# Performance work log

Hardware: AMD Instinct MI355X
Metric: run time of the kernel (lower is better)

Reference implementation:

```python
import jax, jax.numpy as jnp
import numpy as np


def _conv1x1(w, b, x):
    # 1x1 Conv2d == channel matmul: w [O,C], x [B,C,H,W] -> [B,O,H,W]
    return jnp.einsum('oc,bchw->bohw', w, x) + b[None, :, None, None]


def setup_inputs() -> dict:
    key = jax.random.key(0)
    ks = jax.random.split(key, 9)
    C = 512
    B, H, W = 8, 32, 32
    s = 0.02
    return {
        'x': jax.random.normal(ks[0], (B, C, H, W), dtype=jnp.float32),
        'wq': jax.random.normal(ks[1], (C, C), dtype=jnp.float32) * s,
        'bq': jax.random.normal(ks[2], (C,), dtype=jnp.float32) * s,
        'wk': jax.random.normal(ks[3], (C, C), dtype=jnp.float32) * s,
        'bk': jax.random.normal(ks[4], (C,), dtype=jnp.float32) * s,
        'wv': jax.random.normal(ks[5], (C, C), dtype=jnp.float32) * s,
        'bv': jax.random.normal(ks[6], (C,), dtype=jnp.float32) * s,
        'wo': jax.random.normal(ks[7], (C, C), dtype=jnp.float32) * s,
        'bo': jax.random.normal(ks[8], (C,), dtype=jnp.float32) * s,
        'heads': 8,
    }


def reference(x, wq, bq, wk, bk, wv, bv, wo, bo, heads):
    B, C, H, W = x.shape
    N = H * W
    d = C // heads
    scale = jnp.asarray(d, x.dtype) ** 0.5

    vx = _conv1x1(wv, bv, x)                       # value(x), reused for residual
    Q = _conv1x1(wq, bq, x).reshape(B, heads, d, N)
    K = _conv1x1(wk, bk, x).reshape(B, heads, d, N)
    V = vx.reshape(B, heads, d, N)

    attn = jax.nn.softmax(jnp.einsum('bhcn,bhcm->bhnm', Q, K) / scale, axis=-1)
    attn_out = jnp.einsum('bhnm,bhcm->bhcn', attn, V).reshape(B, C, H, W)

    out = attn_out + vx                            # residual uses value(x)
    return _conv1x1(wo, bo, out)
```

## Files before the change

### kernel.cpp

```cpp
#include <hip/hip_runtime.h>
#include <cstdint>
#include <cmath>

#define B_ 8
#define C_ 512
#define N_ 1024
#define H_ 8
#define D_ 64


using u16 = unsigned short;

typedef __bf16 bf16x8 __attribute__((ext_vector_type(8)));
typedef float  f32x4  __attribute__((ext_vector_type(4)));
typedef unsigned short us8 __attribute__((ext_vector_type(8)));

#if __has_builtin(__builtin_amdgcn_exp2f)
#define EXP2(x) __builtin_amdgcn_exp2f(x)
#else
#define EXP2(x) exp2f(x)
#endif

#define QSCALE 0.1803368801111244f


__device__ __forceinline__ float b2f(u16 u) {
    return __uint_as_float(((uint32_t)u) << 16);
}
__device__ __forceinline__ u16 f2b(float f) {
    uint32_t x = __float_as_uint(f);
    return (u16)((x + 0x7fffu + ((x >> 16) & 1u)) >> 16);
}
__device__ __forceinline__ u16 f2bt(float f) {
    return (u16)(__float_as_uint(f) >> 16);
}
__device__ __forceinline__ float sf(float f) {
    return (fabsf(f) < 1e30f) ? f : 0.0f;
}
__device__ __forceinline__ u16 sf2b(float f) { return f2b(sf(f)); }

template<bool WB>
__device__ __forceinline__ us8 ldw(const void* W, size_t idx) {
    if constexpr (WB) {
        return *(const us8*)((const u16*)W + idx);
    } else {
        const float* p = (const float*)W + idx;
        float4 a = *(const float4*)p, b = *(const float4*)(p + 4);
        us8 pk;
        pk[0] = sf2b(a.x); pk[1] = sf2b(a.y); pk[2] = sf2b(a.z); pk[3] = sf2b(a.w);
        pk[4] = sf2b(b.x); pk[5] = sf2b(b.y); pk[6] = sf2b(b.z); pk[7] = sf2b(b.w);
        return pk;
    }
}


__global__ __launch_bounds__(256) void k_pre(const float* __restrict__ x,
                                             u16* __restrict__ xt,
                                             const float* __restrict__ wq,
                                             const float* __restrict__ wk,
                                             const float* __restrict__ wv,
                                             const float* __restrict__ wo,
                                             u16* __restrict__ wb) {
    const int tid = threadIdx.x;
    const int nb = blockIdx.x, cb = blockIdx.y, b = blockIdx.z;
    if (b == 8) {
        if (wb == nullptr) return;
        int base = (cb * 16 + nb) * 256 + tid;
#pragma unroll
        for (int i = 0; i < 8; ++i) {
            int idx = base + i * 32768;
            int m = idx >> 16;
            int off = (idx & 65535) << 2;
            const float* src = (m == 0) ? wq : (m == 1) ? wk : (m == 2) ? wv : wo;
            float4 v = *(const float4*)&src[off];
            ushort4 w;
            w.x = sf2b(v.x); w.y = sf2b(v.y); w.z = sf2b(v.z); w.w = sf2b(v.w);
            *(ushort4*)&wb[(m << 18) + off] = w;
        }
        return;
    }
    __shared__ __align__(16) u16 t[64][72];
#pragma unroll
    for (int i = 0; i < 4; ++i) {
        int q = tid + i * 256;
        int row = q >> 4, cg = q & 15;
        float4 v = *(const float4*)&x[((size_t)(b * C_ + cb * 64 + row) << 10) + nb * 64 + cg * 4];
        ushort4 w;
        w.x = sf2b(v.x); w.y = sf2b(v.y); w.z = sf2b(v.z); w.w = sf2b(v.w);
        *(ushort4*)&t[row][cg * 4] = w;
    }
    __syncthreads();
#pragma unroll
    for (int i = 0; i < 4; ++i) {
        int q = tid + i * 256;
        int nrow = q >> 4, cg = q & 15;
        ushort4 w;
        w.x = t[cg * 4 + 0][nrow];
        w.y = t[cg * 4 + 1][nrow];
        w.z = t[cg * 4 + 2][nrow];
        w.w = t[cg * 4 + 3][nrow];
        *(ushort4*)&xt[((size_t)(b * N_ + nb * 64 + nrow) << 9) + cb * 64 + cg * 4] = w;
    }
}


template<bool WB>
__global__ __launch_bounds__(256) void k_proj_t(
    const u16* __restrict__ xt,
    const void* __restrict__ wq, const float* __restrict__ bq,
    const void* __restrict__ wk, const float* __restrict__ bk,
    const void* __restrict__ wv, const float* __restrict__ bv,
    u16* __restrict__ qt, u16* __restrict__ kt,
    u16* __restrict__ v,  u16* __restrict__ vxt) {
    __shared__ __align__(16) u16 lA[128 * 64];
    __shared__ __align__(16) u16 lB[128 * 64];
    const int tid = threadIdx.x;
    const int op = blockIdx.z >> 3, b = blockIdx.z & 7;
    const int n0 = blockIdx.x * 128, o0 = blockIdx.y * 128;
    const void*  W  = (op == 0) ? wq : (op == 1) ? wk : wv;
    const float* BI = (op == 0) ? bq : (op == 1) ? bk : bv;
    const u16* A = xt + ((size_t)b << 19);
    const int lane = tid & 63, wave = tid >> 6;
    const int wm = (wave >> 1) * 64, wn = (wave & 1) * 64;
    const int l15 = lane & 15, lg = lane >> 4;
    const int xs = (l15 & 7) << 3;

    f32x4 acc[4][4];
    const f32x4 vzero = {0.f, 0.f, 0.f, 0.f};
#pragma unroll
    for (int i = 0; i < 4; ++i)
#pragma unroll
        for (int j = 0; j < 4; ++j) acc[i][j] = vzero;

    us8 ra[4], rwB[4];
    auto loadk = [&](int k0) {
#pragma unroll
        for (int p = 0; p < 4; ++p) {
            int slot = p * 256 + tid;
            int row = slot >> 3, seg = slot & 7;
            ra[p] = *(const us8*)&A[(size_t)(n0 + row) * C_ + k0 + seg * 8];
            rwB[p] = ldw<WB>(W, (size_t)(o0 + row) * C_ + k0 + seg * 8);
        }
    };
    loadk(0);

    for (int k0 = 0; k0 < C_; k0 += 64) {
        __syncthreads();
#pragma unroll
        for (int p = 0; p < 4; ++p) {
            int slot = p * 256 + tid;
            int row = slot >> 3, seg = slot & 7;
            int off = row * 64 + ((seg ^ (row & 7)) << 3);
            *(us8*)&lA[off] = ra[p];
            *(us8*)&lB[off] = rwB[p];
        }
        if (k0 + 64 < C_) loadk(k0 + 64);
        __syncthreads();
#pragma unroll
        for (int kk = 0; kk < 64; kk += 32) {
            const int col = (kk + lg * 8) ^ xs;
            bf16x8 af[4], bfr[4];
#pragma unroll
            for (int i = 0; i < 4; ++i)
                af[i] = *(const bf16x8*)&lA[(wm + i * 16 + l15) * 64 + col];
#pragma unroll
            for (int j = 0; j < 4; ++j)
                bfr[j] = *(const bf16x8*)&lB[(wn + j * 16 + l15) * 64 + col];
#pragma unroll
            for (int i = 0; i < 4; ++i)
#pragma unroll
                for (int j = 0; j < 4; ++j)
                    acc[i][j] = __builtin_amdgcn_mfma_f32_16x16x32_bf16(af[i], bfr[j], acc[i][j], 0, 0, 0);
        }
    }

    if (op < 2) {
        u16* outp = (op == 0) ? qt : kt;
        const float scl = (op == 0) ? QSCALE : 1.0f;
#pragma unroll
        for (int i = 0; i < 4; ++i) {
            int nb2 = n0 + wm + i * 16 + lg * 4;
#pragma unroll
            for (int j = 0; j < 4; ++j) {
                int o = o0 + wn + j * 16 + l15;
                float bias = sf(BI[o]);
                int h = o >> 6, dl = o & 63;
                size_t base = ((size_t)b * H_ + h) << 10;
#pragma unroll
                for (int r = 0; r < 4; ++r)
                    outp[(base + nb2 + r) * D_ + dl] = f2b((acc[i][j][r] + bias) * scl);
            }
        }
    } else {
#pragma unroll
        for (int i = 0; i < 4; ++i) {
            int nb2 = n0 + wm + i * 16 + lg * 4;
#pragma unroll
            for (int j = 0; j < 4; ++j) {
                int o = o0 + wn + j * 16 + l15;
                float bias = sf(BI[o]);
                float p0 = acc[i][j][0] + bias, p1 = acc[i][j][1] + bias;
                float p2 = acc[i][j][2] + bias, p3 = acc[i][j][3] + bias;
                ushort4 pk; pk.x = f2b(p0); pk.y = f2b(p1); pk.z = f2b(p2); pk.w = f2b(p3);
                *(ushort4*)&v[((size_t)(b * C_ + o) << 10) + nb2] = pk;
                vxt[((size_t)(b * N_ + nb2 + 0) << 9) + o] = pk.x;
                vxt[((size_t)(b * N_ + nb2 + 1) << 9) + o] = pk.y;
                vxt[((size_t)(b * N_ + nb2 + 2) << 9) + o] = pk.z;
                vxt[((size_t)(b * N_ + nb2 + 3) << 9) + o] = pk.w;
            }
        }
    }
}


__global__ __launch_bounds__(256, 4) void k_attn(
    const u16* __restrict__ qt, const u16* __restrict__ kt,
    const u16* __restrict__ v,  const u16* __restrict__ vxt,
    u16* __restrict__ rt) {
    __shared__ __align__(16) u16 lK[64 * 64];
    __shared__ __align__(16) u16 lV[64 * 64];
    __shared__ __align__(16) u16 lP[4][32 * 64];
    const int tid = threadIdx.x, lane = tid & 63, wave = tid >> 6;
    const int l15 = lane & 15, lg = lane >> 4;
    const int xs = (l15 & 7) << 3;
    const int bid = blockIdx.x;
    const int qb = bid >> 6, bh = bid & 63;
    const int b = bh >> 3, h = bh & 7;
    const size_t bh_off = (size_t)bh << 16;
    const int q0 = qb * 128;
    const int nA = wave * 32;

    bf16x8 qf[2][2];
#pragma unroll
    for (int nt = 0; nt < 2; ++nt)
#pragma unroll
        for (int k = 0; k < 2; ++k)
            qf[nt][k] = *(const bf16x8*)&qt[bh_off +
                (size_t)(q0 + nA + nt * 16 + l15) * D_ + k * 32 + lg * 8];

    us8 rk[2], rv[2];
    auto loadkv = [&](int mb) {
#pragma unroll
        for (int p = 0; p < 2; ++p) {
            int slot = p * 256 + tid;
            int row = slot >> 3, seg = slot & 7;
            rk[p] = *(const us8*)&kt[bh_off + (size_t)(mb * 64 + row) * D_ + seg * 8];
            rv[p] = *(const us8*)&v[((size_t)(b * C_ + h * 64 + row) << 10) + mb * 64 + seg * 8];
        }
    };
    loadkv(0);

    float L[2] = {0.f, 0.f};
    f32x4 oacc[2][4];
    const f32x4 vzero = {0.f, 0.f, 0.f, 0.f};
#pragma unroll
    for (int nt = 0; nt < 2; ++nt)
#pragma unroll
        for (int ct = 0; ct < 4; ++ct) oacc[nt][ct] = vzero;

    for (int mb = 0; mb < 16; ++mb) {
        __syncthreads();
#pragma unroll
        for (int p = 0; p < 2; ++p) {
            int slot = p * 256 + tid;
            int row = slot >> 3, seg = slot & 7;
            int off = row * 64 + ((seg ^ (row & 7)) << 3);
            *(us8*)&lK[off] = rk[p];
            *(us8*)&lV[off] = rv[p];
        }
        if (mb < 15) loadkv(mb + 1);
        __syncthreads();

        f32x4 s[4][2];
#pragma unroll
        for (int mt = 0; mt < 4; ++mt)
#pragma unroll
            for (int nt = 0; nt < 2; ++nt) s[mt][nt] = vzero;
#pragma unroll
        for (int k = 0; k < 2; ++k) {
            const int col = (k * 32 + lg * 8) ^ xs;
            bf16x8 aK[4];
#pragma unroll
            for (int mt = 0; mt < 4; ++mt)
                aK[mt] = *(const bf16x8*)&lK[(mt * 16 + l15) * 64 + col];
            __builtin_amdgcn_s_setprio(1);
#pragma unroll
            for (int mt = 0; mt < 4; ++mt)
#pragma unroll
                for (int nt = 0; nt < 2; ++nt)
                    s[mt][nt] = __builtin_amdgcn_mfma_f32_16x16x32_bf16(aK[mt], qf[nt][k], s[mt][nt], 0, 0, 0);
            __builtin_amdgcn_s_setprio(0);
        }

#pragma unroll
        for (int mt = 0; mt < 4; ++mt)
#pragma unroll
            for (int nt = 0; nt < 2; ++nt) {
                float p0 = EXP2(s[mt][nt][0]);
                float p1 = EXP2(s[mt][nt][1]);
                float p2 = EXP2(s[mt][nt][2]);
                float p3 = EXP2(s[mt][nt][3]);
                L[nt] += p0 + p1 + p2 + p3;
                ushort4 pk; pk.x = f2bt(p0); pk.y = f2bt(p1); pk.z = f2bt(p2); pk.w = f2bt(p3);
                *(ushort4*)&lP[wave][(nt * 16 + l15) * 64 + ((mt * 16 + lg * 4) ^ xs)] = pk;
            }

#pragma unroll
        for (int kk2 = 0; kk2 < 64; kk2 += 32) {
            const int colv = (kk2 + lg * 8) ^ xs;
            bf16x8 aP[2], bV[4];
#pragma unroll
            for (int nt = 0; nt < 2; ++nt)
                aP[nt] = *(const bf16x8*)&lP[wave][(nt * 16 + l15) * 64 + colv];
#pragma unroll
            for (int ct = 0; ct < 4; ++ct)
                bV[ct] = *(const bf16x8*)&lV[(ct * 16 + l15) * 64 + colv];
            __builtin_amdgcn_s_setprio(1);
#pragma unroll
            for (int nt = 0; nt < 2; ++nt)
#pragma unroll
                for (int ct = 0; ct < 4; ++ct)
                    oacc[nt][ct] = __builtin_amdgcn_mfma_f32_16x16x32_bf16(aP[nt], bV[ct], oacc[nt][ct], 0, 0, 0);
            __builtin_amdgcn_s_setprio(0);
        }
    }

#pragma unroll
    for (int nt = 0; nt < 2; ++nt) {
        float s2 = L[nt];
        s2 += __shfl_xor(s2, 16);
        s2 += __shfl_xor(s2, 32);
        L[nt] = s2;
    }

#pragma unroll
    for (int nt = 0; nt < 2; ++nt) {
        float inv[4];
#pragma unroll
        for (int r = 0; r < 4; ++r) inv[r] = 1.0f / __shfl(L[nt], lg * 4 + r);
#pragma unroll
        for (int ct = 0; ct < 4; ++ct) {
            int ch = h * 64 + ct * 16 + l15;
#pragma unroll
            for (int r = 0; r < 4; ++r) {
                int n = q0 + nA + nt * 16 + lg * 4 + r;
                size_t idx = ((size_t)(b * N_ + n) << 9) + ch;
                rt[idx] = f2b(oacc[nt][ct][r] * inv[r] + b2f(vxt[idx]));
            }
        }
    }
}


template<bool WB>
__global__ __launch_bounds__(256) void k_out_t(
    const u16* __restrict__ rt, const void* __restrict__ wo,
    const float* __restrict__ bo, float* __restrict__ out) {
    __shared__ __align__(16) u16 lA[128 * 64];
    __shared__ __align__(16) u16 lB[128 * 64];
    const int tid = threadIdx.x;
    const int b = blockIdx.z;
    const int n0 = blockIdx.x * 128, o0 = blockIdx.y * 128;
    const u16* Rb = rt + ((size_t)b << 19);
    const int lane = tid & 63, wave = tid >> 6;
    const int wm = (wave >> 1) * 64, wn = (wave & 1) * 64;
    const int l15 = lane & 15, lg = lane >> 4;
    const int xs = (l15 & 7) << 3;

    f32x4 acc[4][4];
    const f32x4 vzero = {0.f, 0.f, 0.f, 0.f};
#pragma unroll
    for (int i = 0; i < 4; ++i)
#pragma unroll
        for (int j = 0; j < 4; ++j) acc[i][j] = vzero;

    us8 rb[4], rwB[4];
    auto loadk = [&](int k0) {
#pragma unroll
        for (int p = 0; p < 4; ++p) {
            int slot = p * 256 + tid;
            int row = slot >> 3, seg = slot & 7;
            rwB[p] = ldw<WB>(wo, (size_t)(o0 + row) * C_ + k0 + seg * 8);
            rb[p] = *(const us8*)&Rb[(size_t)(n0 + row) * C_ + k0 + seg * 8];
        }
    };
    loadk(0);

    for (int k0 = 0; k0 < C_; k0 += 64) {
        __syncthreads();
#pragma unroll
        for (int p = 0; p < 4; ++p) {
            int slot = p * 256 + tid;
            int row = slot >> 3, seg = slot & 7;
            int off = row * 64 + ((seg ^ (row & 7)) << 3);
            *(us8*)&lA[off] = rwB[p];
            *(us8*)&lB[off] = rb[p];
        }
        if (k0 + 64 < C_) loadk(k0 + 64);
        __syncthreads();
#pragma unroll
        for (int kk = 0; kk < 64; kk += 32) {
            const int col = (kk + lg * 8) ^ xs;
            bf16x8 af[4], bfr[4];
#pragma unroll
            for (int i = 0; i < 4; ++i)
                af[i] = *(const bf16x8*)&lA[(wm + i * 16 + l15) * 64 + col];
#pragma unroll
            for (int j = 0; j < 4; ++j)
                bfr[j] = *(const bf16x8*)&lB[(wn + j * 16 + l15) * 64 + col];
#pragma unroll
            for (int i = 0; i < 4; ++i)
#pragma unroll
                for (int j = 0; j < 4; ++j)
                    acc[i][j] = __builtin_amdgcn_mfma_f32_16x16x32_bf16(af[i], bfr[j], acc[i][j], 0, 0, 0);
        }
    }

#pragma unroll
    for (int i = 0; i < 4; ++i) {
#pragma unroll
        for (int j = 0; j < 4; ++j) {
            int nn = n0 + wn + j * 16 + l15;
#pragma unroll
            for (int r = 0; r < 4; ++r) {
                int o = o0 + wm + i * 16 + lg * 4 + r;
                out[((size_t)(b * C_ + o) << 10) + nn] = acc[i][j][r] + sf(bo[o]);
            }
        }
    }
}


extern "C" void kernel_launch(void* const* d_in, const int* in_sizes, int n_in,
                              void* d_out, int out_size, void* d_ws, size_t ws_size,
                              hipStream_t stream) {
    const float* x  = (const float*)d_in[0];
    const float* wq = (const float*)d_in[1];
    const float* bq = (const float*)d_in[2];
    const float* wk = (const float*)d_in[3];
    const float* bk = (const float*)d_in[4];
    const float* wv = (const float*)d_in[5];
    const float* bv = (const float*)d_in[6];
    const float* wo = (const float*)d_in[7];
    const float* bo = (const float*)d_in[8];
    float* out = (float*)d_out;
    u16* ws = (u16*)d_ws;

    const size_t T = (size_t)B_ * C_ * N_;
    const size_t WSZ = (size_t)4 * C_ * C_;
    if (ws_size < 5 * T * sizeof(u16)) return;

    u16* xt  = ws;
    u16* qt  = ws + 1 * T;
    u16* kt  = ws + 2 * T;
    u16* vv  = ws + 3 * T;
    u16* vxt = ws + 4 * T;
    u16* rt  = xt;
    u16* wb  = ws + 5 * T;

    const bool wbfit = ws_size >= (5 * T + WSZ) * sizeof(u16);

    k_pre<<<dim3(16, 8, 9), 256, 0, stream>>>(x, xt, wq, wk, wv, wo,
                                              wbfit ? wb : (u16*)nullptr);
    if (wbfit) {
        k_proj_t<true><<<dim3(8, 4, 24), 256, 0, stream>>>(
            xt, wb, bq, wb + 262144, bk, wb + 524288, bv, qt, kt, vv, vxt);
    } else {
        k_proj_t<false><<<dim3(8, 4, 24), 256, 0, stream>>>(
            xt, wq, bq, wk, bk, wv, bv, qt, kt, vv, vxt);
    }
    k_attn<<<dim3(512), 256, 0, stream>>>(qt, kt, vv, vxt, rt);
    if (wbfit) {
        k_out_t<true><<<dim3(8, 4, 8), 256, 0, stream>>>(rt, wb + 786432, bo, out);
    } else {
        k_out_t<false><<<dim3(8, 4, 8), 256, 0, stream>>>(rt, wo, bo, out);
    }
}
```

Before: 78.99 us.

## Use direct global-to-LDS loads and double-buffer K/V tiles in attention

Replaces register-staged global loads and LDS stores with global_load_lds direct-to-LDS transfers in the projection GEMMs (bf16 weight path) and the attention kernel. The swizzle is moved into the global source address. The attention kernel double-buffers K/V tiles so the next block is fetched while the current one is computed, with one barrier per iteration. Occupancy is lowered to 3 blocks per CU to fit the extra LDS. The GEMM bf16 path loses its register prefetch overlap, since the load is issued and waited on within the same iteration.

```diff
diff --git a/kernel.cpp b/kernel.cpp
--- a/kernel.cpp
+++ b/kernel.cpp
@@ -39,18 +39,20 @@
 }
 __device__ __forceinline__ u16 sf2b(float f) { return f2b(sf(f)); }
 
-template<bool WB>
-__device__ __forceinline__ us8 ldw(const void* W, size_t idx) {
-    if constexpr (WB) {
-        return *(const us8*)((const u16*)W + idx);
-    } else {
-        const float* p = (const float*)W + idx;
-        float4 a = *(const float4*)p, b = *(const float4*)(p + 4);
-        us8 pk;
-        pk[0] = sf2b(a.x); pk[1] = sf2b(a.y); pk[2] = sf2b(a.z); pk[3] = sf2b(a.w);
-        pk[4] = sf2b(b.x); pk[5] = sf2b(b.y); pk[6] = sf2b(b.z); pk[7] = sf2b(b.w);
-        return pk;
-    }
+__device__ __forceinline__ void gl16(const void* g, const void* l) {
+    __builtin_amdgcn_global_load_lds(
+        (const __attribute__((address_space(1))) uint32_t*)g,
+        (__attribute__((address_space(3))) uint32_t*)(uint32_t)(uintptr_t)l,
+        16, 0, 0);
+}
+
+__device__ __forceinline__ us8 ldwf(const float* W, size_t idx) {
+    const float* p = W + idx;
+    float4 a = *(const float4*)p, b = *(const float4*)(p + 4);
+    us8 pk;
+    pk[0] = sf2b(a.x); pk[1] = sf2b(a.y); pk[2] = sf2b(a.z); pk[3] = sf2b(a.w);
+    pk[4] = sf2b(b.x); pk[5] = sf2b(b.y); pk[6] = sf2b(b.z); pk[7] = sf2b(b.w);
+    return pk;
 }
 
 
@@ -139,22 +141,35 @@
             int slot = p * 256 + tid;
             int row = slot >> 3, seg = slot & 7;
             ra[p] = *(const us8*)&A[(size_t)(n0 + row) * C_ + k0 + seg * 8];
-            rwB[p] = ldw<WB>(W, (size_t)(o0 + row) * C_ + k0 + seg * 8);
+            rwB[p] = ldwf((const float*)W, (size_t)(o0 + row) * C_ + k0 + seg * 8);
         }
     };
-    loadk(0);
+    if constexpr (!WB) loadk(0);
 
     for (int k0 = 0; k0 < C_; k0 += 64) {
         __syncthreads();
-#pragma unroll
-        for (int p = 0; p < 4; ++p) {
-            int slot = p * 256 + tid;
-            int row = slot >> 3, seg = slot & 7;
-            int off = row * 64 + ((seg ^ (row & 7)) << 3);
-            *(us8*)&lA[off] = ra[p];
-            *(us8*)&lB[off] = rwB[p];
-        }
-        if (k0 + 64 < C_) loadk(k0 + 64);
+        if constexpr (WB) {
+            const u16* W16 = (const u16*)W;
+#pragma unroll
+            for (int p = 0; p < 4; ++p) {
+                int slot = p * 256 + tid;
+                int row = slot >> 3;
+                int segs = (slot & 7) ^ (row & 7);
+                int lb = (p * 256 + (tid & 192)) * 8;
+                gl16(&A[(size_t)(n0 + row) * C_ + k0 + segs * 8], &lA[lb]);
+                gl16(&W16[(size_t)(o0 + row) * C_ + k0 + segs * 8], &lB[lb]);
+            }
+        } else {
+#pragma unroll
+            for (int p = 0; p < 4; ++p) {
+                int slot = p * 256 + tid;
+                int row = slot >> 3, seg = slot & 7;
+                int off = row * 64 + ((seg ^ (row & 7)) << 3);
+                *(us8*)&lA[off] = ra[p];
+                *(us8*)&lB[off] = rwB[p];
+            }
+            if (k0 + 64 < C_) loadk(k0 + 64);
+        }
         __syncthreads();
 #pragma unroll
         for (int kk = 0; kk < 64; kk += 32) {
@@ -213,12 +228,12 @@
 }
 
 
-__global__ __launch_bounds__(256, 4) void k_attn(
+__global__ __launch_bounds__(256, 3) void k_attn(
     const u16* __restrict__ qt, const u16* __restrict__ kt,
     const u16* __restrict__ v,  const u16* __restrict__ vxt,
     u16* __restrict__ rt) {
-    __shared__ __align__(16) u16 lK[64 * 64];
-    __shared__ __align__(16) u16 lV[64 * 64];
+    __shared__ __align__(16) u16 lK[2][64 * 64];
+    __shared__ __align__(16) u16 lV[2][64 * 64];
     __shared__ __align__(16) u16 lP[4][32 * 64];
     const int tid = threadIdx.x, lane = tid & 63, wave = tid >> 6;
     const int l15 = lane & 15, lg = lane >> 4;
@@ -238,17 +253,19 @@
             qf[nt][k] = *(const bf16x8*)&qt[bh_off +
                 (size_t)(q0 + nA + nt * 16 + l15) * D_ + k * 32 + lg * 8];
 
-    us8 rk[2], rv[2];
-    auto loadkv = [&](int mb) {
+    auto stage = [&](int mb, int buf) {
 #pragma unroll
         for (int p = 0; p < 2; ++p) {
             int slot = p * 256 + tid;
-            int row = slot >> 3, seg = slot & 7;
-            rk[p] = *(const us8*)&kt[bh_off + (size_t)(mb * 64 + row) * D_ + seg * 8];
-            rv[p] = *(const us8*)&v[((size_t)(b * C_ + h * 64 + row) << 10) + mb * 64 + seg * 8];
+            int row = slot >> 3;
+            int segs = (slot & 7) ^ (row & 7);
+            int lb = (p * 256 + (tid & 192)) * 8;
+            gl16(&kt[bh_off + (size_t)(mb * 64 + row) * D_ + segs * 8], &lK[buf][lb]);
+            gl16(&v[((size_t)(b * C_ + h * 64 + row) << 10) + mb * 64 + segs * 8], &lV[buf][lb]);
         }
     };
-    loadkv(0);
+    stage(0, 0);
+    __syncthreads();
 
     float L[2] = {0.f, 0.f};
     f32x4 oacc[2][4];
@@ -259,17 +276,10 @@
         for (int ct = 0; ct < 4; ++ct) oacc[nt][ct] = vzero;
 
     for (int mb = 0; mb < 16; ++mb) {
-        __syncthreads();
-#pragma unroll
-        for (int p = 0; p < 2; ++p) {
-            int slot = p * 256 + tid;
-            int row = slot >> 3, seg = slot & 7;
-            int off = row * 64 + ((seg ^ (row & 7)) << 3);
-            *(us8*)&lK[off] = rk[p];
-            *(us8*)&lV[off] = rv[p];
-        }
-        if (mb < 15) loadkv(mb + 1);
-        __syncthreads();
+        const int cur = mb & 1;
+        if (mb < 15) stage(mb + 1, cur ^ 1);
+        const u16* lKc = lK[cur];
+        const u16* lVc = lV[cur];
 
         f32x4 s[4][2];
 #pragma unroll
@@ -282,7 +292,7 @@
             bf16x8 aK[4];
 #pragma unroll
             for (int mt = 0; mt < 4; ++mt)
-                aK[mt] = *(const bf16x8*)&lK[(mt * 16 + l15) * 64 + col];
+                aK[mt] = *(const bf16x8*)&lKc[(mt * 16 + l15) * 64 + col];
             __builtin_amdgcn_s_setprio(1);
 #pragma unroll
             for (int mt = 0; mt < 4; ++mt)
@@ -314,7 +324,7 @@
                 aP[nt] = *(const bf16x8*)&lP[wave][(nt * 16 + l15) * 64 + colv];
 #pragma unroll
             for (int ct = 0; ct < 4; ++ct)
-                bV[ct] = *(const bf16x8*)&lV[(ct * 16 + l15) * 64 + colv];
+                bV[ct] = *(const bf16x8*)&lVc[(ct * 16 + l15) * 64 + colv];
             __builtin_amdgcn_s_setprio(1);
 #pragma unroll
             for (int nt = 0; nt < 2; ++nt)
@@ -323,6 +333,8 @@
                     oacc[nt][ct] = __builtin_amdgcn_mfma_f32_16x16x32_bf16(aP[nt], bV[ct], oacc[nt][ct], 0, 0, 0);
             __builtin_amdgcn_s_setprio(0);
         }
+
+        __syncthreads();
     }
 
 #pragma unroll
@@ -380,23 +392,36 @@
         for (int p = 0; p < 4; ++p) {
             int slot = p * 256 + tid;
             int row = slot >> 3, seg = slot & 7;
-            rwB[p] = ldw<WB>(wo, (size_t)(o0 + row) * C_ + k0 + seg * 8);
+            rwB[p] = ldwf((const float*)wo, (size_t)(o0 + row) * C_ + k0 + seg * 8);
             rb[p] = *(const us8*)&Rb[(size_t)(n0 + row) * C_ + k0 + seg * 8];
         }
     };
-    loadk(0);
+    if constexpr (!WB) loadk(0);
 
     for (int k0 = 0; k0 < C_; k0 += 64) {
         __syncthreads();
-#pragma unroll
-        for (int p = 0; p < 4; ++p) {
-            int slot = p * 256 + tid;
-            int row = slot >> 3, seg = slot & 7;
-            int off = row * 64 + ((seg ^ (row & 7)) << 3);
-            *(us8*)&lA[off] = rwB[p];
-            *(us8*)&lB[off] = rb[p];
-        }
-        if (k0 + 64 < C_) loadk(k0 + 64);
+        if constexpr (WB) {
+            const u16* W16 = (const u16*)wo;
+#pragma unroll
+            for (int p = 0; p < 4; ++p) {
+                int slot = p * 256 + tid;
+                int row = slot >> 3;
+                int segs = (slot & 7) ^ (row & 7);
+                int lb = (p * 256 + (tid & 192)) * 8;
+                gl16(&W16[(size_t)(o0 + row) * C_ + k0 + segs * 8], &lA[lb]);
+                gl16(&Rb[(size_t)(n0 + row) * C_ + k0 + segs * 8], &lB[lb]);
+            }
+        } else {
+#pragma unroll
+            for (int p = 0; p < 4; ++p) {
+                int slot = p * 256 + tid;
+                int row = slot >> 3, seg = slot & 7;
+                int off = row * 64 + ((seg ^ (row & 7)) << 3);
+                *(us8*)&lA[off] = rwB[p];
+                *(us8*)&lB[off] = rb[p];
+            }
+            if (k0 + 64 < C_) loadk(k0 + 64);
+        }
         __syncthreads();
 #pragma unroll
         for (int kk = 0; kk < 64; kk += 32) {
```

New measurement: 76.31 us. 1.04x faster.

## Drop transposed V copy, read K/V directly from global, vectorize output stores

Applied to the files above, without the earlier changes.

Removes the separate transposed value buffer (vxt) and its scattered 2-byte stores in the projection kernel, reading the residual from the channel-major V buffer instead. The attention kernel stops staging K and V tiles through shared memory with barriers and loads MFMA fragments straight from global memory, relying on cache reuse across the four waves. The output projection swaps operand roles so each lane writes a contiguous float4 per channel instead of scalar strided stores. Dropping the LDS staging removes syncs and LDS traffic but makes every wave issue its own global loads for K/V, which may raise latency exposure.

```diff
diff --git a/kernel.cpp b/kernel.cpp
--- a/kernel.cpp
+++ b/kernel.cpp
@@ -111,7 +111,7 @@
     const void* __restrict__ wk, const float* __restrict__ bk,
     const void* __restrict__ wv, const float* __restrict__ bv,
     u16* __restrict__ qt, u16* __restrict__ kt,
-    u16* __restrict__ v,  u16* __restrict__ vxt) {
+    u16* __restrict__ v) {
     __shared__ __align__(16) u16 lA[128 * 64];
     __shared__ __align__(16) u16 lB[128 * 64];
     const int tid = threadIdx.x;
@@ -199,26 +199,21 @@
             for (int j = 0; j < 4; ++j) {
                 int o = o0 + wn + j * 16 + l15;
                 float bias = sf(BI[o]);
-                float p0 = acc[i][j][0] + bias, p1 = acc[i][j][1] + bias;
-                float p2 = acc[i][j][2] + bias, p3 = acc[i][j][3] + bias;
-                ushort4 pk; pk.x = f2b(p0); pk.y = f2b(p1); pk.z = f2b(p2); pk.w = f2b(p3);
+                ushort4 pk;
+                pk.x = f2b(acc[i][j][0] + bias);
+                pk.y = f2b(acc[i][j][1] + bias);
+                pk.z = f2b(acc[i][j][2] + bias);
+                pk.w = f2b(acc[i][j][3] + bias);
                 *(ushort4*)&v[((size_t)(b * C_ + o) << 10) + nb2] = pk;
-                vxt[((size_t)(b * N_ + nb2 + 0) << 9) + o] = pk.x;
-                vxt[((size_t)(b * N_ + nb2 + 1) << 9) + o] = pk.y;
-                vxt[((size_t)(b * N_ + nb2 + 2) << 9) + o] = pk.z;
-                vxt[((size_t)(b * N_ + nb2 + 3) << 9) + o] = pk.w;
             }
         }
     }
 }
 
 
-__global__ __launch_bounds__(256, 4) void k_attn(
+__global__ __launch_bounds__(256) void k_attn(
     const u16* __restrict__ qt, const u16* __restrict__ kt,
-    const u16* __restrict__ v,  const u16* __restrict__ vxt,
-    u16* __restrict__ rt) {
-    __shared__ __align__(16) u16 lK[64 * 64];
-    __shared__ __align__(16) u16 lV[64 * 64];
+    const u16* __restrict__ v, u16* __restrict__ rt) {
     __shared__ __align__(16) u16 lP[4][32 * 64];
     const int tid = threadIdx.x, lane = tid & 63, wave = tid >> 6;
     const int l15 = lane & 15, lg = lane >> 4;
@@ -238,17 +233,8 @@
             qf[nt][k] = *(const bf16x8*)&qt[bh_off +
                 (size_t)(q0 + nA + nt * 16 + l15) * D_ + k * 32 + lg * 8];
 
-    us8 rk[2], rv[2];
-    auto loadkv = [&](int mb) {
-#pragma unroll
-        for (int p = 0; p < 2; ++p) {
-            int slot = p * 256 + tid;
-            int row = slot >> 3, seg = slot & 7;
-            rk[p] = *(const us8*)&kt[bh_off + (size_t)(mb * 64 + row) * D_ + seg * 8];
-            rv[p] = *(const us8*)&v[((size_t)(b * C_ + h * 64 + row) << 10) + mb * 64 + seg * 8];
-        }
-    };
-    loadkv(0);
+    const u16* Kb = kt + bh_off;
+    const u16* Vb = v + ((size_t)(b * C_ + h * 64) << 10);
 
     float L[2] = {0.f, 0.f};
     f32x4 oacc[2][4];
@@ -259,18 +245,6 @@
         for (int ct = 0; ct < 4; ++ct) oacc[nt][ct] = vzero;
 
     for (int mb = 0; mb < 16; ++mb) {
-        __syncthreads();
-#pragma unroll
-        for (int p = 0; p < 2; ++p) {
-            int slot = p * 256 + tid;
-            int row = slot >> 3, seg = slot & 7;
-            int off = row * 64 + ((seg ^ (row & 7)) << 3);
-            *(us8*)&lK[off] = rk[p];
-            *(us8*)&lV[off] = rv[p];
-        }
-        if (mb < 15) loadkv(mb + 1);
-        __syncthreads();
-
         f32x4 s[4][2];
 #pragma unroll
         for (int mt = 0; mt < 4; ++mt)
@@ -278,11 +252,10 @@
             for (int nt = 0; nt < 2; ++nt) s[mt][nt] = vzero;
 #pragma unroll
         for (int k = 0; k < 2; ++k) {
-            const int col = (k * 32 + lg * 8) ^ xs;
             bf16x8 aK[4];
 #pragma unroll
             for (int mt = 0; mt < 4; ++mt)
-                aK[mt] = *(const bf16x8*)&lK[(mt * 16 + l15) * 64 + col];
+                aK[mt] = *(const bf16x8*)&Kb[(size_t)(mb * 64 + mt * 16 + l15) * D_ + k * 32 + lg * 8];
             __builtin_amdgcn_s_setprio(1);
 #pragma unroll
             for (int mt = 0; mt < 4; ++mt)
@@ -314,7 +287,7 @@
                 aP[nt] = *(const bf16x8*)&lP[wave][(nt * 16 + l15) * 64 + colv];
 #pragma unroll
             for (int ct = 0; ct < 4; ++ct)
-                bV[ct] = *(const bf16x8*)&lV[(ct * 16 + l15) * 64 + colv];
+                bV[ct] = *(const bf16x8*)&Vb[((size_t)(ct * 16 + l15) << 10) + mb * 64 + kk2 + lg * 8];
             __builtin_amdgcn_s_setprio(1);
 #pragma unroll
             for (int nt = 0; nt < 2; ++nt)
@@ -341,11 +314,13 @@
 #pragma unroll
         for (int ct = 0; ct < 4; ++ct) {
             int ch = h * 64 + ct * 16 + l15;
+            int nbase = q0 + nA + nt * 16 + lg * 4;
+            ushort4 rv = *(const ushort4*)&v[((size_t)(b * C_ + ch) << 10) + nbase];
+            const u16 rvv[4] = {rv.x, rv.y, rv.z, rv.w};
 #pragma unroll
             for (int r = 0; r < 4; ++r) {
-                int n = q0 + nA + nt * 16 + lg * 4 + r;
-                size_t idx = ((size_t)(b * N_ + n) << 9) + ch;
-                rt[idx] = f2b(oacc[nt][ct][r] * inv[r] + b2f(vxt[idx]));
+                size_t idx = ((size_t)(b * N_ + nbase + r) << 9) + ch;
+                rt[idx] = f2b(oacc[nt][ct][r] * inv[r] + b2f(rvv[r]));
             }
         }
     }
@@ -374,14 +349,14 @@
 #pragma unroll
         for (int j = 0; j < 4; ++j) acc[i][j] = vzero;
 
-    us8 rb[4], rwB[4];
+    us8 ra[4], rwB[4];
     auto loadk = [&](int k0) {
 #pragma unroll
         for (int p = 0; p < 4; ++p) {
             int slot = p * 256 + tid;
             int row = slot >> 3, seg = slot & 7;
+            ra[p] = *(const us8*)&Rb[(size_t)(n0 + row) * C_ + k0 + seg * 8];
             rwB[p] = ldw<WB>(wo, (size_t)(o0 + row) * C_ + k0 + seg * 8);
-            rb[p] = *(const us8*)&Rb[(size_t)(n0 + row) * C_ + k0 + seg * 8];
         }
     };
     loadk(0);
@@ -393,8 +368,8 @@
             int slot = p * 256 + tid;
             int row = slot >> 3, seg = slot & 7;
             int off = row * 64 + ((seg ^ (row & 7)) << 3);
-            *(us8*)&lA[off] = rwB[p];
-            *(us8*)&lB[off] = rb[p];
+            *(us8*)&lA[off] = ra[p];
+            *(us8*)&lB[off] = rwB[p];
         }
         if (k0 + 64 < C_) loadk(k0 + 64);
         __syncthreads();
@@ -418,14 +393,17 @@
 
 #pragma unroll
     for (int i = 0; i < 4; ++i) {
+        int nb2 = n0 + wm + i * 16 + lg * 4;
 #pragma unroll
         for (int j = 0; j < 4; ++j) {
-            int nn = n0 + wn + j * 16 + l15;
-#pragma unroll
-            for (int r = 0; r < 4; ++r) {
-                int o = o0 + wm + i * 16 + lg * 4 + r;
-                out[((size_t)(b * C_ + o) << 10) + nn] = acc[i][j][r] + sf(bo[o]);
-            }
+            int o = o0 + wn + j * 16 + l15;
+            float bias = sf(bo[o]);
+            float4 st;
+            st.x = acc[i][j][0] + bias;
+            st.y = acc[i][j][1] + bias;
+            st.z = acc[i][j][2] + bias;
+            st.w = acc[i][j][3] + bias;
+            *(float4*)&out[((size_t)(b * C_ + o) << 10) + nb2] = st;
         }
     }
 }
@@ -454,7 +432,6 @@
     u16* qt  = ws + 1 * T;
     u16* kt  = ws + 2 * T;
     u16* vv  = ws + 3 * T;
-    u16* vxt = ws + 4 * T;
     u16* rt  = xt;
     u16* wb  = ws + 5 * T;
 
@@ -464,12 +441,12 @@
                                               wbfit ? wb : (u16*)nullptr);
     if (wbfit) {
         k_proj_t<true><<<dim3(8, 4, 24), 256, 0, stream>>>(
-            xt, wb, bq, wb + 262144, bk, wb + 524288, bv, qt, kt, vv, vxt);
+            xt, wb, bq, wb + 262144, bk, wb + 524288, bv, qt, kt, vv);
     } else {
         k_proj_t<false><<<dim3(8, 4, 24), 256, 0, stream>>>(
-            xt, wq, bq, wk, bk, wv, bv, qt, kt, vv, vxt);
-    }
-    k_attn<<<dim3(512), 256, 0, stream>>>(qt, kt, vv, vxt, rt);
+            xt, wq, bq, wk, bk, wv, bv, qt, kt, vv);
+    }
+    k_attn<<<dim3(512), 256, 0, stream>>>(qt, kt, vv, rt);
     if (wbfit) {
         k_out_t<true><<<dim3(8, 4, 8), 256, 0, stream>>>(rt, wb + 786432, bo, out);
     } else {
```

New measurement: 107.1 us. 1.36x slower.
